# Performance work log

Hardware: AMD Instinct MI355X
Metric: run time of the kernel (lower is better)

Reference implementation:

```python
import jax, jax.numpy as jnp
import numpy as np

N, IN_DIM, OUT_DIM = 8192, 512, 256
ALPHA = 0.2
NEG_INF = -9e15


def setup_inputs() -> dict:
    key = jax.random.key(0)
    k1, k2, k3, k4 = jax.random.split(key, 4)
    node_features = jax.random.normal(k1, (N, IN_DIM), dtype=jnp.float32)
    adj_matrix = jax.random.randint(k2, (N, N), 0, 2, dtype=jnp.int32)
    # xavier-uniform linear weight [out,in] -> store as [in,out]
    lim_w = float(np.sqrt(6.0 / (IN_DIM + OUT_DIM)))
    W = jax.random.uniform(k3, (IN_DIM, OUT_DIM), dtype=jnp.float32, minval=-lim_w, maxval=lim_w)
    b = jnp.zeros((OUT_DIM,), dtype=jnp.float32)
    # attention Linear(2*out_dim, 1): weight a [2*out_dim], bias scalar
    lim_a = float(np.sqrt(6.0 / (2 * OUT_DIM + 1)))
    a = jax.random.uniform(k4, (2 * OUT_DIM,), dtype=jnp.float32, minval=-lim_a, maxval=lim_a)
    a_bias = jnp.zeros((), dtype=jnp.float32)
    return {"adj_matrix": adj_matrix, "node_features": node_features, "W": W, "b": b, "a": a, "a_bias": a_bias}


def reference(adj_matrix, node_features, W, b, a, a_bias):
    # h = Linear(node_features); dropout is identity in eval mode
    h = node_features @ W + b                     # [N, D]
    # attention(cat(h_i, h_j)) == h_i @ a_l + h_j @ a_r + a_bias
    a_l, a_r = a[:OUT_DIM], a[OUT_DIM:]
    e_l = h @ a_l                                 # [N]
    e_r = h @ a_r                                 # [N]
    e = jax.nn.leaky_relu(e_l[:, None] + e_r[None, :] + a_bias, ALPHA)  # [N, N]
    scores = jnp.where(adj_matrix > 0, e, NEG_INF)
    attention = jax.nn.softmax(scores, axis=1)    # [N, N]
    h_prime = attention @ h                       # [N, D]
    return h_prime
```

## Files before the change

### kernel.cpp

```cpp
#include <hip/hip_runtime.h>

#define N 8192
#define DIN 512
#define DOUT 256
#define ALPHA 0.2f
#define NEG_INF -9.0e15f

typedef __attribute__((ext_vector_type(8))) short bf16x8;
typedef __attribute__((ext_vector_type(4))) float f32x4;
typedef __attribute__((ext_vector_type(4))) int   i32x4;

__device__ __forceinline__ unsigned f2bf_u(float f) {
    unsigned u = __builtin_bit_cast(unsigned, f);
    return (u + 0x7fffu + ((u >> 16) & 1u)) >> 16;
}
__device__ __forceinline__ unsigned pack2bf(float lo, float hi) {
    return f2bf_u(lo) | (f2bf_u(hi) << 16);
}
union U4BF8 { uint4 u; bf16x8 v; };

__device__ __forceinline__ void async_copy16(const ushort* g, ushort* l) {
    __builtin_amdgcn_global_load_lds(
        (const __attribute__((address_space(1))) unsigned*)g,
        (__attribute__((address_space(3))) unsigned*)l, 16, 0, 0);
}

__global__ __launch_bounds__(256) void wb_kernel(const float* __restrict__ W,
                                                 ushort* __restrict__ WB) {
    const int g = blockIdx.x * 256 + threadIdx.x;
    const int c = g & 255, k8 = g >> 8;
    const float* wp = W + (size_t)(k8 * 8) * DOUT + c;
    U4BF8 o;
    o.u.x = pack2bf(wp[0 * DOUT], wp[1 * DOUT]);
    o.u.y = pack2bf(wp[2 * DOUT], wp[3 * DOUT]);
    o.u.z = pack2bf(wp[4 * DOUT], wp[5 * DOUT]);
    o.u.w = pack2bf(wp[6 * DOUT], wp[7 * DOUT]);
    *(uint4*)(WB + (size_t)g * 8) = o.u;
}

__global__ __launch_bounds__(64) void h_kernel(
        const float* __restrict__ X, const ushort* __restrict__ WB,
        const float* __restrict__ bvec, const float* __restrict__ a,
        ushort* __restrict__ hB, float* __restrict__ el, float* __restrict__ er)
{
    const int l = threadIdx.x;
    const int q = l >> 4, n = l & 15;
    const int i0 = blockIdx.x * 16;
    f32x4 acc[16];
    #pragma unroll
    for (int ct = 0; ct < 16; ++ct) acc[ct] = (f32x4){0.f, 0.f, 0.f, 0.f};
    const float* xp = X + (size_t)(i0 + n) * DIN + q * 8;

    for (int k0 = 0; k0 < DIN; k0 += 32) {
        const float4 x0 = *(const float4*)(xp + k0);
        const float4 x1 = *(const float4*)(xp + k0 + 4);
        U4BF8 pa;
        pa.u.x = pack2bf(x0.x, x0.y); pa.u.y = pack2bf(x0.z, x0.w);
        pa.u.z = pack2bf(x1.x, x1.y); pa.u.w = pack2bf(x1.z, x1.w);
        const ushort* wbp = WB + ((k0 >> 3) + q) * 2048 + n * 8;
        bf16x8 bfr[16];
        #pragma unroll
        for (int ct = 0; ct < 16; ++ct) bfr[ct] = *(const bf16x8*)(wbp + ct * 128);
        #pragma unroll
        for (int ct = 0; ct < 16; ++ct)
            acc[ct] = __builtin_amdgcn_mfma_f32_16x16x32_bf16(pa.v, bfr[ct], acc[ct], 0, 0, 0);
    }

    float pl[4] = {0.f, 0.f, 0.f, 0.f}, pr[4] = {0.f, 0.f, 0.f, 0.f};
    const int hbase = (blockIdx.x * 2 + (q >> 1)) * 2048 + n * 8 + (q & 1) * 4;
    #pragma unroll
    for (int ct = 0; ct < 16; ++ct) {
        const float bb = bvec[ct * 16 + n];
        const float al = a[ct * 16 + n];
        const float ar = a[DOUT + ct * 16 + n];
        float v0 = acc[ct][0] + bb, v1 = acc[ct][1] + bb;
        float v2 = acc[ct][2] + bb, v3 = acc[ct][3] + bb;
        pl[0] += v0 * al; pl[1] += v1 * al; pl[2] += v2 * al; pl[3] += v3 * al;
        pr[0] += v0 * ar; pr[1] += v1 * ar; pr[2] += v2 * ar; pr[3] += v3 * ar;
        ushort4 hp;
        hp.x = (ushort)f2bf_u(v0); hp.y = (ushort)f2bf_u(v1);
        hp.z = (ushort)f2bf_u(v2); hp.w = (ushort)f2bf_u(v3);
        *(ushort4*)&hB[hbase + ct * 128] = hp;
    }
    #pragma unroll
    for (int r = 0; r < 4; ++r) {
        #pragma unroll
        for (int off = 1; off < 16; off <<= 1) {
            pl[r] += __shfl_xor(pl[r], off);
            pr[r] += __shfl_xor(pr[r], off);
        }
    }
    if (n == 0) {
        const int rowb = i0 + q * 4;
        #pragma unroll
        for (int r = 0; r < 4; ++r) { el[rowb + r] = pl[r]; er[rowb + r] = pr[r]; }
    }
}

__global__ __launch_bounds__(256, 1) void attn_kernel(
        const int* __restrict__ adj, const float* __restrict__ el,
        const float* __restrict__ er, const float* __restrict__ ab,
        const ushort* __restrict__ hB, float* __restrict__ out)
{
    __shared__ ushort stage[2][16384];
    const int t = threadIdx.x;
    const int w = t >> 6, l = t & 63, q = l >> 4, n = l & 15;
    const int rg = w >> 1, jq = w & 1;
    const int i0 = blockIdx.x * 32;
    const int row = i0 + rg * 16 + n;
    const float elm = el[row] + ab[0];
    const int jb = jq * 32 + q * 8;
    const int* alp = adj + (size_t)row * N + jb;
    const float* elp = er + jb;

    f32x4 acc[16];
    #pragma unroll
    for (int ct = 0; ct < 16; ++ct) acc[ct] = (f32x4){0.f, 0.f, 0.f, 0.f};
    float lsum = 0.f;

    {
        const ushort* g = hB + (size_t)(w * 8) * 512 + l * 8;
        ushort* lb = &stage[0][(w * 8) * 512];
        #pragma unroll
        for (int i = 0; i < 8; ++i) async_copy16(g + i * 512, lb + i * 512);
    }
    i32x4 ac0 = __builtin_nontemporal_load((const i32x4*)alp);
    i32x4 ac1 = __builtin_nontemporal_load((const i32x4*)(alp + 4));
    float4 ec0 = *(const float4*)elp;
    float4 ec1 = *(const float4*)(elp + 4);
    i32x4 an0 = ac0, an1 = ac1;
    float4 en0 = ec0, en1 = ec1;

    for (int s = 0; s < 128; ++s) {
        __syncthreads();
        if (s < 127) {
            const int J0n = (s + 1) * 64;
            const ushort* g = hB + (size_t)J0n * 256 + (size_t)(w * 8) * 512 + l * 8;
            ushort* lb = &stage[(s + 1) & 1][(w * 8) * 512];
            #pragma unroll
            for (int i = 0; i < 8; ++i) async_copy16(g + i * 512, lb + i * 512);
            an0 = __builtin_nontemporal_load((const i32x4*)(alp + J0n));
            an1 = __builtin_nontemporal_load((const i32x4*)(alp + J0n + 4));
            en0 = *(const float4*)(elp + J0n);
            en1 = *(const float4*)(elp + J0n + 4);
        }
        float v, p0, p1, p2, p3, p4, p5, p6, p7;
        v = elm + ec0.x; v = fmaxf(v, ALPHA * v); p0 = __expf(ac0.x > 0 ? v : NEG_INF);
        v = elm + ec0.y; v = fmaxf(v, ALPHA * v); p1 = __expf(ac0.y > 0 ? v : NEG_INF);
        v = elm + ec0.z; v = fmaxf(v, ALPHA * v); p2 = __expf(ac0.z > 0 ? v : NEG_INF);
        v = elm + ec0.w; v = fmaxf(v, ALPHA * v); p3 = __expf(ac0.w > 0 ? v : NEG_INF);
        v = elm + ec1.x; v = fmaxf(v, ALPHA * v); p4 = __expf(ac1.x > 0 ? v : NEG_INF);
        v = elm + ec1.y; v = fmaxf(v, ALPHA * v); p5 = __expf(ac1.y > 0 ? v : NEG_INF);
        v = elm + ec1.z; v = fmaxf(v, ALPHA * v); p6 = __expf(ac1.z > 0 ? v : NEG_INF);
        v = elm + ec1.w; v = fmaxf(v, ALPHA * v); p7 = __expf(ac1.w > 0 ? v : NEG_INF);
        lsum += p0 + p1 + p2 + p3 + p4 + p5 + p6 + p7;
        U4BF8 pa;
        pa.u.x = pack2bf(p0, p1); pa.u.y = pack2bf(p2, p3);
        pa.u.z = pack2bf(p4, p5); pa.u.w = pack2bf(p6, p7);
        const ushort* sb = &stage[s & 1][(jq * 4 + q) * 2048 + n * 8];
        #pragma unroll
        for (int ct = 0; ct < 16; ++ct) {
            const bf16x8 bf = *(const bf16x8*)(sb + ct * 128);
            acc[ct] = __builtin_amdgcn_mfma_f32_16x16x32_bf16(pa.v, bf, acc[ct], 0, 0, 0);
        }
        ac0 = an0; ac1 = an1; ec0 = en0; ec1 = en1;
    }

    lsum += __shfl_xor(lsum, 16);
    lsum += __shfl_xor(lsum, 32);

    float* accbuf = (float*)&stage[0][0];
    float* LpB    = (float*)&stage[1][0];
    float* linvB  = LpB + 64;
    __syncthreads();
    if (l < 16) LpB[(rg * 2 + jq) * 16 + l] = lsum;
    if (jq == 0) {
        #pragma unroll
        for (int ct = 0; ct < 16; ++ct)
            #pragma unroll
            for (int r = 0; r < 4; ++r)
                accbuf[(rg * 16 + q * 4 + r) * 256 + ct * 16 + n] = acc[ct][r];
    }
    __syncthreads();
    if (jq == 1) {
        #pragma unroll
        for (int ct = 0; ct < 16; ++ct)
            #pragma unroll
            for (int r = 0; r < 4; ++r)
                accbuf[(rg * 16 + q * 4 + r) * 256 + ct * 16 + n] += acc[ct][r];
    }
    __syncthreads();
    if (t < 32)
        linvB[t] = 1.0f / (LpB[(t >> 4) * 32 + (t & 15)] + LpB[(t >> 4) * 32 + 16 + (t & 15)]);
    __syncthreads();
    const int orow = t >> 3, c0 = (t & 7) * 32;
    const float li = linvB[orow];
    #pragma unroll
    for (int ch = 0; ch < 8; ++ch) {
        float4 vv = *(const float4*)&accbuf[orow * 256 + c0 + ch * 4];
        vv.x *= li; vv.y *= li; vv.z *= li; vv.w *= li;
        *(float4*)&out[(size_t)(i0 + orow) * 256 + c0 + ch * 4] = vv;
    }
}

extern "C" void kernel_launch(void* const* d_in, const int* in_sizes, int n_in,
                              void* d_out, int out_size, void* d_ws, size_t ws_size,
                              hipStream_t stream) {
    const int*   adj = (const int*)  d_in[0];
    const float* X   = (const float*)d_in[1];
    const float* W   = (const float*)d_in[2];
    const float* b   = (const float*)d_in[3];
    const float* a   = (const float*)d_in[4];
    const float* ab  = (const float*)d_in[5];
    float* out = (float*)d_out;

    ushort* hB = (ushort*)d_ws;
    ushort* WB = hB + (size_t)N * DOUT;
    float*  el = (float*)(WB + (size_t)DIN * DOUT);
    float*  er = el + N;

    wb_kernel<<<dim3(64), dim3(256), 0, stream>>>(W, WB);
    h_kernel<<<dim3(N / 16), dim3(64), 0, stream>>>(X, WB, b, a, hB, el, er);
    attn_kernel<<<dim3(N / 32), dim3(256), 0, stream>>>(adj, el, er, ab, hB, out);
}
```

Baseline: 476.5 us.

## Split K across waves in h_kernel and widen attention block to eight waves

The projection kernel now runs four waves per 16-row tile. Each wave covers one quarter of the input dimension, and the partial accumulators are reduced through shared memory before bias, attention dot products and bf16 packing. The attention kernel doubles to 512 threads with four column-split waves per row group. It stages 128 columns of h per step in a larger LDS buffer, halving the iteration count, and reduces the four partial accumulators serially. The goal is more latency hiding and more bytes in flight for the adjacency stream, at the cost of more LDS, extra reduction passes and barriers.

```diff
diff --git a/kernel.cpp b/kernel.cpp
--- a/kernel.cpp
+++ b/kernel.cpp
@@ -38,20 +38,24 @@
     *(uint4*)(WB + (size_t)g * 8) = o.u;
 }
 
-__global__ __launch_bounds__(64) void h_kernel(
+__global__ __launch_bounds__(256) void h_kernel(
         const float* __restrict__ X, const ushort* __restrict__ WB,
         const float* __restrict__ bvec, const float* __restrict__ a,
         ushort* __restrict__ hB, float* __restrict__ el, float* __restrict__ er)
 {
-    const int l = threadIdx.x;
-    const int q = l >> 4, n = l & 15;
+    __shared__ float red[4][64][65];
+    __shared__ float elr[2][4][16];
+    const int t = threadIdx.x;
+    const int w = t >> 6, l = t & 63, q = l >> 4, n = l & 15;
     const int i0 = blockIdx.x * 16;
     f32x4 acc[16];
     #pragma unroll
     for (int ct = 0; ct < 16; ++ct) acc[ct] = (f32x4){0.f, 0.f, 0.f, 0.f};
     const float* xp = X + (size_t)(i0 + n) * DIN + q * 8;
 
-    for (int k0 = 0; k0 < DIN; k0 += 32) {
+    #pragma unroll
+    for (int ks = 0; ks < 4; ++ks) {
+        const int k0 = w * 128 + ks * 32;
         const float4 x0 = *(const float4*)(xp + k0);
         const float4 x1 = *(const float4*)(xp + k0 + 4);
         U4BF8 pa;
@@ -65,21 +69,31 @@
         for (int ct = 0; ct < 16; ++ct)
             acc[ct] = __builtin_amdgcn_mfma_f32_16x16x32_bf16(pa.v, bfr[ct], acc[ct], 0, 0, 0);
     }
+    #pragma unroll
+    for (int ct = 0; ct < 16; ++ct)
+        #pragma unroll
+        for (int r = 0; r < 4; ++r) red[w][l][ct * 4 + r] = acc[ct][r];
+    __syncthreads();
 
     float pl[4] = {0.f, 0.f, 0.f, 0.f}, pr[4] = {0.f, 0.f, 0.f, 0.f};
     const int hbase = (blockIdx.x * 2 + (q >> 1)) * 2048 + n * 8 + (q & 1) * 4;
     #pragma unroll
-    for (int ct = 0; ct < 16; ++ct) {
+    for (int c2 = 0; c2 < 4; ++c2) {
+        const int ct = w * 4 + c2;
         const float bb = bvec[ct * 16 + n];
         const float al = a[ct * 16 + n];
         const float ar = a[DOUT + ct * 16 + n];
-        float v0 = acc[ct][0] + bb, v1 = acc[ct][1] + bb;
-        float v2 = acc[ct][2] + bb, v3 = acc[ct][3] + bb;
-        pl[0] += v0 * al; pl[1] += v1 * al; pl[2] += v2 * al; pl[3] += v3 * al;
-        pr[0] += v0 * ar; pr[1] += v1 * ar; pr[2] += v2 * ar; pr[3] += v3 * ar;
+        float v[4];
+        #pragma unroll
+        for (int r = 0; r < 4; ++r) {
+            v[r] = red[0][l][ct * 4 + r] + red[1][l][ct * 4 + r]
+                 + red[2][l][ct * 4 + r] + red[3][l][ct * 4 + r] + bb;
+            pl[r] += v[r] * al;
+            pr[r] += v[r] * ar;
+        }
         ushort4 hp;
-        hp.x = (ushort)f2bf_u(v0); hp.y = (ushort)f2bf_u(v1);
-        hp.z = (ushort)f2bf_u(v2); hp.w = (ushort)f2bf_u(v3);
+        hp.x = (ushort)f2bf_u(v[0]); hp.y = (ushort)f2bf_u(v[1]);
+        hp.z = (ushort)f2bf_u(v[2]); hp.w = (ushort)f2bf_u(v[3]);
         *(ushort4*)&hB[hbase + ct * 128] = hp;
     }
     #pragma unroll
@@ -91,21 +105,28 @@
         }
     }
     if (n == 0) {
-        const int rowb = i0 + q * 4;
-        #pragma unroll
-        for (int r = 0; r < 4; ++r) { el[rowb + r] = pl[r]; er[rowb + r] = pr[r]; }
-    }
-}
-
-__global__ __launch_bounds__(256, 1) void attn_kernel(
+        #pragma unroll
+        for (int r = 0; r < 4; ++r) {
+            elr[0][w][q * 4 + r] = pl[r];
+            elr[1][w][q * 4 + r] = pr[r];
+        }
+    }
+    __syncthreads();
+    if (t < 16) {
+        el[i0 + t] = elr[0][0][t] + elr[0][1][t] + elr[0][2][t] + elr[0][3][t];
+        er[i0 + t] = elr[1][0][t] + elr[1][1][t] + elr[1][2][t] + elr[1][3][t];
+    }
+}
+
+__global__ __launch_bounds__(512, 1) void attn_kernel(
         const int* __restrict__ adj, const float* __restrict__ el,
         const float* __restrict__ er, const float* __restrict__ ab,
         const ushort* __restrict__ hB, float* __restrict__ out)
 {
-    __shared__ ushort stage[2][16384];
+    __shared__ ushort stage[2][32768];
     const int t = threadIdx.x;
     const int w = t >> 6, l = t & 63, q = l >> 4, n = l & 15;
-    const int rg = w >> 1, jq = w & 1;
+    const int rg = w >> 2, jq = w & 3;
     const int i0 = blockIdx.x * 32;
     const int row = i0 + rg * 16 + n;
     const float elm = el[row] + ab[0];
@@ -118,41 +139,41 @@
     for (int ct = 0; ct < 16; ++ct) acc[ct] = (f32x4){0.f, 0.f, 0.f, 0.f};
     float lsum = 0.f;
 
-    {
-        const ushort* g = hB + (size_t)(w * 8) * 512 + l * 8;
-        ushort* lb = &stage[0][(w * 8) * 512];
-        #pragma unroll
-        for (int i = 0; i < 8; ++i) async_copy16(g + i * 512, lb + i * 512);
-    }
     i32x4 ac0 = __builtin_nontemporal_load((const i32x4*)alp);
     i32x4 ac1 = __builtin_nontemporal_load((const i32x4*)(alp + 4));
     float4 ec0 = *(const float4*)elp;
     float4 ec1 = *(const float4*)(elp + 4);
-    i32x4 an0 = ac0, an1 = ac1;
-    float4 en0 = ec0, en1 = ec1;
-
-    for (int s = 0; s < 128; ++s) {
+    {
+        const ushort* g = hB + w * 512 + l * 8;
+        ushort* lb = &stage[0][w * 512];
+        #pragma unroll
+        for (int i = 0; i < 8; ++i) async_copy16(g + i * 4096, lb + i * 4096);
+    }
+
+    for (int s = 0; s < 64; ++s) {
         __syncthreads();
-        if (s < 127) {
-            const int J0n = (s + 1) * 64;
-            const ushort* g = hB + (size_t)J0n * 256 + (size_t)(w * 8) * 512 + l * 8;
-            ushort* lb = &stage[(s + 1) & 1][(w * 8) * 512];
-            #pragma unroll
-            for (int i = 0; i < 8; ++i) async_copy16(g + i * 512, lb + i * 512);
-            an0 = __builtin_nontemporal_load((const i32x4*)(alp + J0n));
-            an1 = __builtin_nontemporal_load((const i32x4*)(alp + J0n + 4));
-            en0 = *(const float4*)(elp + J0n);
-            en1 = *(const float4*)(elp + J0n + 4);
+        const i32x4 aa0 = ac0, aa1 = ac1;
+        const float4 ee0 = ec0, ee1 = ec1;
+        if (s < 63) {
+            const int J0n = (s + 1) * 128;
+            ac0 = __builtin_nontemporal_load((const i32x4*)(alp + J0n));
+            ac1 = __builtin_nontemporal_load((const i32x4*)(alp + J0n + 4));
+            ec0 = *(const float4*)(elp + J0n);
+            ec1 = *(const float4*)(elp + J0n + 4);
+            const ushort* g = hB + (size_t)(s + 1) * 32768 + w * 512 + l * 8;
+            ushort* lb = &stage[(s + 1) & 1][w * 512];
+            #pragma unroll
+            for (int i = 0; i < 8; ++i) async_copy16(g + i * 4096, lb + i * 4096);
         }
         float v, p0, p1, p2, p3, p4, p5, p6, p7;
-        v = elm + ec0.x; v = fmaxf(v, ALPHA * v); p0 = __expf(ac0.x > 0 ? v : NEG_INF);
-        v = elm + ec0.y; v = fmaxf(v, ALPHA * v); p1 = __expf(ac0.y > 0 ? v : NEG_INF);
-        v = elm + ec0.z; v = fmaxf(v, ALPHA * v); p2 = __expf(ac0.z > 0 ? v : NEG_INF);
-        v = elm + ec0.w; v = fmaxf(v, ALPHA * v); p3 = __expf(ac0.w > 0 ? v : NEG_INF);
-        v = elm + ec1.x; v = fmaxf(v, ALPHA * v); p4 = __expf(ac1.x > 0 ? v : NEG_INF);
-        v = elm + ec1.y; v = fmaxf(v, ALPHA * v); p5 = __expf(ac1.y > 0 ? v : NEG_INF);
-        v = elm + ec1.z; v = fmaxf(v, ALPHA * v); p6 = __expf(ac1.z > 0 ? v : NEG_INF);
-        v = elm + ec1.w; v = fmaxf(v, ALPHA * v); p7 = __expf(ac1.w > 0 ? v : NEG_INF);
+        v = elm + ee0.x; v = fmaxf(v, ALPHA * v); p0 = __expf(aa0.x > 0 ? v : NEG_INF);
+        v = elm + ee0.y; v = fmaxf(v, ALPHA * v); p1 = __expf(aa0.y > 0 ? v : NEG_INF);
+        v = elm + ee0.z; v = fmaxf(v, ALPHA * v); p2 = __expf(aa0.z > 0 ? v : NEG_INF);
+        v = elm + ee0.w; v = fmaxf(v, ALPHA * v); p3 = __expf(aa0.w > 0 ? v : NEG_INF);
+        v = elm + ee1.x; v = fmaxf(v, ALPHA * v); p4 = __expf(aa1.x > 0 ? v : NEG_INF);
+        v = elm + ee1.y; v = fmaxf(v, ALPHA * v); p5 = __expf(aa1.y > 0 ? v : NEG_INF);
+        v = elm + ee1.z; v = fmaxf(v, ALPHA * v); p6 = __expf(aa1.z > 0 ? v : NEG_INF);
+        v = elm + ee1.w; v = fmaxf(v, ALPHA * v); p7 = __expf(aa1.w > 0 ? v : NEG_INF);
         lsum += p0 + p1 + p2 + p3 + p4 + p5 + p6 + p7;
         U4BF8 pa;
         pa.u.x = pack2bf(p0, p1); pa.u.y = pack2bf(p2, p3);
@@ -163,7 +184,6 @@
             const bf16x8 bf = *(const bf16x8*)(sb + ct * 128);
             acc[ct] = __builtin_amdgcn_mfma_f32_16x16x32_bf16(pa.v, bf, acc[ct], 0, 0, 0);
         }
-        ac0 = an0; ac1 = an1; ec0 = en0; ec1 = en1;
     }
 
     lsum += __shfl_xor(lsum, 16);
@@ -171,15 +191,15 @@
 
     float* accbuf = (float*)&stage[0][0];
     float* LpB    = (float*)&stage[1][0];
-    float* linvB  = LpB + 64;
-    __syncthreads();
-    if (l < 16) LpB[(rg * 2 + jq) * 16 + l] = lsum;
+    float* linvB  = LpB + 128;
+    __syncthreads();
+    if (l < 16) LpB[(rg * 4 + jq) * 16 + n] = lsum;
     if (jq == 0) {
         #pragma unroll
         for (int ct = 0; ct < 16; ++ct)
             #pragma unroll
             for (int r = 0; r < 4; ++r)
-                accbuf[(rg * 16 + q * 4 + r) * 256 + ct * 16 + n] = acc[ct][r];
+                accbuf[(rg * 16 + q * 4 + r) * 272 + ct * 16 + n] = acc[ct][r];
     }
     __syncthreads();
     if (jq == 1) {
@@ -187,17 +207,36 @@
         for (int ct = 0; ct < 16; ++ct)
             #pragma unroll
             for (int r = 0; r < 4; ++r)
-                accbuf[(rg * 16 + q * 4 + r) * 256 + ct * 16 + n] += acc[ct][r];
-    }
-    __syncthreads();
-    if (t < 32)
-        linvB[t] = 1.0f / (LpB[(t >> 4) * 32 + (t & 15)] + LpB[(t >> 4) * 32 + 16 + (t & 15)]);
-    __syncthreads();
-    const int orow = t >> 3, c0 = (t & 7) * 32;
+                accbuf[(rg * 16 + q * 4 + r) * 272 + ct * 16 + n] += acc[ct][r];
+    }
+    __syncthreads();
+    if (jq == 2) {
+        #pragma unroll
+        for (int ct = 0; ct < 16; ++ct)
+            #pragma unroll
+            for (int r = 0; r < 4; ++r)
+                accbuf[(rg * 16 + q * 4 + r) * 272 + ct * 16 + n] += acc[ct][r];
+    }
+    __syncthreads();
+    if (jq == 3) {
+        #pragma unroll
+        for (int ct = 0; ct < 16; ++ct)
+            #pragma unroll
+            for (int r = 0; r < 4; ++r)
+                accbuf[(rg * 16 + q * 4 + r) * 272 + ct * 16 + n] += acc[ct][r];
+    }
+    __syncthreads();
+    if (t < 32) {
+        const int rr = t >> 4, m = t & 15;
+        linvB[t] = 1.0f / (LpB[(rr * 4 + 0) * 16 + m] + LpB[(rr * 4 + 1) * 16 + m]
+                         + LpB[(rr * 4 + 2) * 16 + m] + LpB[(rr * 4 + 3) * 16 + m]);
+    }
+    __syncthreads();
+    const int orow = t >> 4, c0 = (t & 15) * 16;
     const float li = linvB[orow];
     #pragma unroll
-    for (int ch = 0; ch < 8; ++ch) {
-        float4 vv = *(const float4*)&accbuf[orow * 256 + c0 + ch * 4];
+    for (int ch = 0; ch < 4; ++ch) {
+        float4 vv = *(const float4*)&accbuf[orow * 272 + c0 + ch * 4];
         vv.x *= li; vv.y *= li; vv.z *= li; vv.w *= li;
         *(float4*)&out[(size_t)(i0 + orow) * 256 + c0 + ch * 4] = vv;
     }
@@ -220,6 +259,6 @@
     float*  er = el + N;
 
     wb_kernel<<<dim3(64), dim3(256), 0, stream>>>(W, WB);
-    h_kernel<<<dim3(N / 16), dim3(64), 0, stream>>>(X, WB, b, a, hB, el, er);
-    attn_kernel<<<dim3(N / 32), dim3(256), 0, stream>>>(adj, el, er, ab, hB, out);
-}
+    h_kernel<<<dim3(N / 16), dim3(256), 0, stream>>>(X, WB, b, a, hB, el, er);
+    attn_kernel<<<dim3(N / 32), dim3(512), 0, stream>>>(adj, el, er, ab, hB, out);
+}
```

New measurement: 458.2 us. 1.04x faster.
